# Performance work log

Hardware: AMD Instinct MI355X
Metric: run time of the kernel (lower is better)

The kernel has to match this reference:

```python
import jax, jax.numpy as jnp
import numpy as np


def setup_inputs() -> dict:
    key = jax.random.key(0)
    ks = jax.random.split(key, 5)
    B, S, D, L = 16, 256, 768, 32
    return {
        "head": jax.random.normal(ks[0], (B, S, D), dtype=jnp.float32),
        "dep": jax.random.normal(ks[1], (B, S, D), dtype=jnp.float32),
        "label_U_diag": jax.random.normal(ks[2], (L, D), dtype=jnp.float32) * 0.02,
        "label_W": jax.random.normal(ks[3], (L, 2 * D), dtype=jnp.float32) * 0.02,
        "label_b": jax.random.normal(ks[4], (L,), dtype=jnp.float32) * 0.02,
    }


def reference(head, dep, label_U_diag, label_W, label_b):
    # head, dep: [b, s, d]; label_U_diag: [l, d]; label_W: [l, 2d]; label_b: [l]
    d = head.shape[-1]
    # Bilinear term with diagonal U: t1[b,l,i,o] = sum_d head[b,i,d]*U[l,d]*dep[b,o,d]
    t1 = jnp.einsum('bid,ld,bod->blio', head, label_U_diag, dep)
    # Linear term: W @ concat(head_i, dep_o) = W_h @ head_i + W_d @ dep_o
    W_h, W_d = label_W[:, :d], label_W[:, d:]
    t2_h = jnp.einsum('ld,bid->bli', W_h, head)  # [b, l, s]
    t2_d = jnp.einsum('ld,bod->blo', W_d, dep)   # [b, l, s]
    return t1 + t2_h[:, :, :, None] + t2_d[:, :, None, :] + label_b[None, :, None, None]
```

## Files before the change

kernel.cpp:

```cpp
#include <hip/hip_runtime.h>
#include <hip/hip_bf16.h>
#include <stdint.h>


#define B_ 16
#define S_ 256
#define D_ 768
#define L_ 32
#define KQ_ (D_ / 8)
#define NT_ 24

typedef unsigned short ushort_t;
typedef __attribute__((ext_vector_type(4))) float f32x4;
typedef __attribute__((ext_vector_type(8))) short s16x8;

__device__ __forceinline__ unsigned int pack_bf16(float f0, float f1) {
  unsigned int u0 = __builtin_bit_cast(unsigned int, f0) + 0x8000u;
  unsigned int u1 = __builtin_bit_cast(unsigned int, f1) + 0x8000u;
  return __builtin_amdgcn_perm(u1, u0, 0x07060302);
}

__global__ __launch_bounds__(256) void prep_kernel(
    const float* __restrict__ head, const float* __restrict__ dep,
    const float* __restrict__ labelW, ushort_t* __restrict__ depb,
    float* __restrict__ t2h, float* __restrict__ t2d) {
  const int wave = threadIdx.x >> 6;
  const int lane = threadIdx.x & 63;
  const int g = blockIdx.x * 4 + wave;
  const int sel = g >> 10;
  const int idx = g & 1023;
  const int b = idx >> 6;
  const int row0 = (idx & 63) * 4;
  const float* src = sel ? dep : head;
  float* t2x = sel ? t2d : t2h;
  const int d0 = lane * 12;

  float h[4][12];
  const float* rp = src + ((size_t)(b * S_ + row0)) * D_ + d0;
#pragma unroll
  for (int r = 0; r < 4; ++r) {
    float4 v0 = *(const float4*)(rp + (size_t)r * D_);
    float4 v1 = *(const float4*)(rp + (size_t)r * D_ + 4);
    float4 v2 = *(const float4*)(rp + (size_t)r * D_ + 8);
    h[r][0] = v0.x; h[r][1] = v0.y; h[r][2] = v0.z; h[r][3] = v0.w;
    h[r][4] = v1.x; h[r][5] = v1.y; h[r][6] = v1.z; h[r][7] = v1.w;
    h[r][8] = v2.x; h[r][9] = v2.y; h[r][10] = v2.z; h[r][11] = v2.w;
  }
  if (sel) {
    const size_t bb = (size_t)b * (KQ_ * S_ * 8);
    const int m = lane >> 1;
#pragma unroll
    for (int r = 0; r < 4; ++r) {
      const int col = row0 + r;
      unsigned int q0 = pack_bf16(h[r][0], h[r][1]);
      unsigned int q1 = pack_bf16(h[r][2], h[r][3]);
      unsigned int q2 = pack_bf16(h[r][4], h[r][5]);
      unsigned int q3 = pack_bf16(h[r][6], h[r][7]);
      unsigned int q4 = pack_bf16(h[r][8], h[r][9]);
      unsigned int q5 = pack_bf16(h[r][10], h[r][11]);
      if ((lane & 1) == 0) {
        uint4 a = {q0, q1, q2, q3};
        uint2 c = {q4, q5};
        *(uint4*)(depb + bb + ((size_t)(3 * m) * S_ + col) * 8) = a;
        *(uint2*)(depb + bb + ((size_t)(3 * m + 1) * S_ + col) * 8) = c;
      } else {
        uint2 c = {q0, q1};
        uint4 a = {q2, q3, q4, q5};
        *(uint2*)(depb + bb + ((size_t)(3 * m + 1) * S_ + col) * 8 + 4) = c;
        *(uint4*)(depb + bb + ((size_t)(3 * m + 2) * S_ + col) * 8) = a;
      }
    }
  }
  const float* wbase = labelW + sel * D_ + d0;
  for (int c = 0; c < 2; ++c) {
    float v[64];
#pragma unroll
    for (int j = 0; j < 64; ++j) v[j] = 0.f;
    const float* wc = wbase + (size_t)(c * 16) * (2 * D_);
#pragma unroll
    for (int lq = 0; lq < 16; ++lq) {
      const float* wp = wc + (size_t)lq * (2 * D_);
      float4 w0 = *(const float4*)(wp);
      float4 w1 = *(const float4*)(wp + 4);
      float4 w2 = *(const float4*)(wp + 8);
      float w[12] = {w0.x, w0.y, w0.z, w0.w, w1.x, w1.y, w1.z, w1.w,
                     w2.x, w2.y, w2.z, w2.w};
#pragma unroll
      for (int j = 0; j < 12; ++j) {
        v[lq * 4 + 0] += h[0][j] * w[j];
        v[lq * 4 + 1] += h[1][j] * w[j];
        v[lq * 4 + 2] += h[2][j] * w[j];
        v[lq * 4 + 3] += h[3][j] * w[j];
      }
    }
#pragma unroll
    for (int off = 32; off >= 1; off >>= 1) {
      const bool hi = (lane & off) != 0;
#pragma unroll
      for (int k = 0; k < 64; ++k) {
        if (k >= off) continue;
        float send = hi ? v[k] : v[k + off];
        float keep = hi ? v[k + off] : v[k];
        v[k] = keep + __shfl_xor(send, off);
      }
    }
    t2x[((size_t)(b * L_ + c * 16 + (lane >> 2))) * S_ + row0 + (lane & 3)] =
        v[0];
  }
}


#define SWZ(o) ((o) ^ ((((o) >> 10) & 3) << 4))

__global__ __launch_bounds__(256, 3) void main_kernel(
    const float* __restrict__ head, const ushort_t* __restrict__ depb,
    const float* __restrict__ U, const float* __restrict__ bias,
    const float* __restrict__ t2h, const float* __restrict__ t2d,
    float* __restrict__ out) {
  __shared__ __attribute__((aligned(16))) ushort_t As[2 * 128 * 32];
  __shared__ float T2[256];

  const int hw = blockIdx.x;
  const int bid = ((hw & 7) << 8) | (hw >> 3);
  const int oh = bid & 1;
  const int ih = (bid >> 1) & 1;
  const int l = (bid >> 2) & (L_ - 1);
  const int b = bid >> 7;
  const int ti = ih * 128;
  const int to = oh * 128;
  const int t = threadIdx.x;
  const int lane = t & 63;
  const int wave = t >> 6;
  const int m_base = (wave >> 1) * 64;
  const int n_base = (wave & 1) * 64;

  for (int i = t; i < 256; i += 256)
    T2[i] = (i < 128) ? t2h[((size_t)(b * L_ + l)) * S_ + ti + i]
                      : t2d[((size_t)(b * L_ + l)) * S_ + to + (i - 128)];
  const float bv = bias[l];

  const int row0 = t >> 2;
  const int kg = t & 3;
  const float* hp0 = head + ((size_t)(b * S_ + ti + row0)) * D_ + kg * 8;
  const float* hp1 = hp0 + (size_t)64 * D_;
  const float* Up = U + (size_t)l * D_ + kg * 8;
  const int awo0s = SWZ((kg * 128 + row0) * 8);
  const int awo1s = awo0s + 512;

  const int aros = SWZ(((lane >> 4) * 128 + m_base + (lane & 15)) * 8);

  const ushort_t* dfb =
      depb + (size_t)b * (KQ_ * S_ * 8) +
      ((size_t)((lane >> 4) * 256 + to + n_base + (lane & 15))) * 8;

  f32x4 acc[4][4];
#pragma unroll
  for (int i = 0; i < 4; ++i)
#pragma unroll
    for (int j = 0; j < 4; ++j) acc[i][j] = {0.f, 0.f, 0.f, 0.f};

  s16x8 bfA[4], bfB[4];

  {
    float4 h0 = *(const float4*)(hp0);
    float4 h1 = *(const float4*)(hp0 + 4);
    float4 h2 = *(const float4*)(hp1);
    float4 h3 = *(const float4*)(hp1 + 4);
    float4 u0 = *(const float4*)(Up);
    float4 u1 = *(const float4*)(Up + 4);
    uint4 w0, w1;
    w0.x = pack_bf16(h0.x * u0.x, h0.y * u0.y);
    w0.y = pack_bf16(h0.z * u0.z, h0.w * u0.w);
    w0.z = pack_bf16(h1.x * u1.x, h1.y * u1.y);
    w0.w = pack_bf16(h1.z * u1.z, h1.w * u1.w);
    w1.x = pack_bf16(h2.x * u0.x, h2.y * u0.y);
    w1.y = pack_bf16(h2.z * u0.z, h2.w * u0.w);
    w1.z = pack_bf16(h3.x * u1.x, h3.y * u1.y);
    w1.w = pack_bf16(h3.z * u1.z, h3.w * u1.w);
    *(uint4*)(As + awo0s) = w0;
    *(uint4*)(As + awo1s) = w1;
#pragma unroll
    for (int ct = 0; ct < 4; ++ct)
      bfA[ct] = *(const s16x8*)(dfb + ct * 128);
  }
  asm volatile("s_waitcnt lgkmcnt(0)" ::: "memory");
  __builtin_amdgcn_s_barrier();
  __builtin_amdgcn_sched_barrier(0);

#define ITER(PB, BFC, BFN, tcur)                                              \
  {                                                                           \
    int tn = (tcur) + 1;                                                      \
    if (tn == NT_) tn = 0;     \
    const float* hA = hp0 + tn * 32;                                          \
    const float* hB = hp1 + tn * 32;                                          \
    const float* uA = Up + tn * 32;                                           \
    float4 h0 = *(const float4*)(hA);                                         \
    float4 h1 = *(const float4*)(hA + 4);                                     \
    float4 h2 = *(const float4*)(hB);                                         \
    float4 h3 = *(const float4*)(hB + 4);                                     \
    float4 u0 = *(const float4*)(uA);                                         \
    float4 u1 = *(const float4*)(uA + 4);                                     \
    const ushort_t* dfn = dfb + (size_t)tn * 8192;                            \
    _Pragma("unroll") for (int ct = 0; ct < 4; ++ct)                          \
        BFN[ct] = *(const s16x8*)(dfn + ct * 128);                            \
    __builtin_amdgcn_sched_barrier(0);       \
    s16x8 af[4];                                                              \
    _Pragma("unroll") for (int rt = 0; rt < 4; ++rt)                          \
        af[rt] = *(const s16x8*)(As + (PB)*4096 + aros + rt * 128);           \
    _Pragma("unroll") for (int rt = 0; rt < 4; ++rt)                          \
      _Pragma("unroll") for (int ct = 0; ct < 4; ++ct)                        \
          acc[rt][ct] = __builtin_amdgcn_mfma_f32_16x16x32_bf16(              \
              af[rt], BFC[ct], acc[rt][ct], 0, 0, 0);                         \
    uint4 w0, w1;                                                             \
    w0.x = pack_bf16(h0.x * u0.x, h0.y * u0.y);                               \
    w0.y = pack_bf16(h0.z * u0.z, h0.w * u0.w);                               \
    w0.z = pack_bf16(h1.x * u1.x, h1.y * u1.y);                               \
    w0.w = pack_bf16(h1.z * u1.z, h1.w * u1.w);                               \
    w1.x = pack_bf16(h2.x * u0.x, h2.y * u0.y);                               \
    w1.y = pack_bf16(h2.z * u0.z, h2.w * u0.w);                               \
    w1.z = pack_bf16(h3.x * u1.x, h3.y * u1.y);                               \
    w1.w = pack_bf16(h3.z * u1.z, h3.w * u1.w);                               \
    ushort_t* aw = As + ((PB) ^ 1) * 4096;                                    \
    *(uint4*)(aw + awo0s) = w0;                                               \
    *(uint4*)(aw + awo1s) = w1;                                               \
    asm volatile("s_waitcnt lgkmcnt(0)" ::: "memory");                        \
    __builtin_amdgcn_s_barrier();                                             \
    __builtin_amdgcn_sched_barrier(0);                                        \
  }

  for (int tt = 0; tt < NT_; tt += 2) {
    ITER(0, bfA, bfB, tt);
    ITER(1, bfB, bfA, tt + 1);
  }
#undef ITER

  const int colg = lane & 15;
  const int rgrp = lane >> 4;
  float* ob = out + (((size_t)(b * L_ + l)) * S_ + ti) * S_ + to;
#pragma unroll
  for (int rt = 0; rt < 4; ++rt) {
    const int r0 = m_base + rt * 16 + rgrp * 4;
#pragma unroll
    for (int ct = 0; ct < 4; ++ct) {
      const int c = n_base + ct * 16 + colg;
      const float addc = T2[128 + c] + bv;
      float* p = ob + (size_t)r0 * S_ + c;
#pragma unroll
      for (int r = 0; r < 4; ++r)
        p[(size_t)r * S_] = acc[rt][ct][r] + T2[r0 + r] + addc;
    }
  }
}

extern "C" void kernel_launch(void* const* d_in, const int* in_sizes, int n_in,
                              void* d_out, int out_size, void* d_ws, size_t ws_size,
                              hipStream_t stream) {
  const float* head = (const float*)d_in[0];
  const float* dep = (const float*)d_in[1];
  const float* U = (const float*)d_in[2];
  const float* W = (const float*)d_in[3];
  const float* bias = (const float*)d_in[4];
  float* out = (float*)d_out;

  ushort_t* depb = (ushort_t*)d_ws;
  float* t2h = (float*)((char*)d_ws + (size_t)B_ * S_ * D_ * 2);
  float* t2d = t2h + (size_t)B_ * L_ * S_;

  prep_kernel<<<512, 256, 0, stream>>>(head, dep, W, depb, t2h, t2d);
  main_kernel<<<B_ * L_ * 4, 256, 0, stream>>>(head, depb, U, bias, t2h, t2d, out);
}
```

Baseline: 232.9 us.

## Retile main kernel to 64x256 blocks with three k-chunks per barrier

The block tile changes from 128x128 to 64 rows by 256 columns, so all four waves share one 64-row A tile and each wave covers its own 64-column strip of dep. Each shared buffer now holds three 32-wide k-chunks, so a block synchronises 8 times instead of 24, and the head/U prefetch runs three chunks ahead. The aim is fewer barriers and less staging of head*U per output. The cost is more dep traffic per block and a larger shared-memory footprint, with the swizzle adjusted to the new row count.

Result: faster. 224.9 us (-3.4%).

```diff
diff --git a/kernel.cpp b/kernel.cpp
--- a/kernel.cpp
+++ b/kernel.cpp
@@ -8,7 +8,8 @@
 #define D_ 768
 #define L_ 32
 #define KQ_ (D_ / 8)
-#define NT_ 24
+#define NT_ 8
+#define NKT_ 24
 
 typedef unsigned short ushort_t;
 typedef __attribute__((ext_vector_type(4))) float f32x4;
@@ -110,48 +111,42 @@
 }
 
 
-#define SWZ(o) ((o) ^ ((((o) >> 10) & 3) << 4))
+#define SWZ(o) ((o) ^ ((((o) >> 9) & 3) << 4))
 
 __global__ __launch_bounds__(256, 3) void main_kernel(
     const float* __restrict__ head, const ushort_t* __restrict__ depb,
     const float* __restrict__ U, const float* __restrict__ bias,
     const float* __restrict__ t2h, const float* __restrict__ t2d,
     float* __restrict__ out) {
-  __shared__ __attribute__((aligned(16))) ushort_t As[2 * 128 * 32];
-  __shared__ float T2[256];
+  __shared__ __attribute__((aligned(16))) ushort_t As[2 * 3 * 2048];
+  __shared__ float T2[320];
 
   const int hw = blockIdx.x;
   const int bid = ((hw & 7) << 8) | (hw >> 3);
-  const int oh = bid & 1;
-  const int ih = (bid >> 1) & 1;
+  const int rq = bid & 3;
   const int l = (bid >> 2) & (L_ - 1);
   const int b = bid >> 7;
-  const int ti = ih * 128;
-  const int to = oh * 128;
+  const int ti = rq * 64;
   const int t = threadIdx.x;
   const int lane = t & 63;
   const int wave = t >> 6;
-  const int m_base = (wave >> 1) * 64;
-  const int n_base = (wave & 1) * 64;
-
-  for (int i = t; i < 256; i += 256)
-    T2[i] = (i < 128) ? t2h[((size_t)(b * L_ + l)) * S_ + ti + i]
-                      : t2d[((size_t)(b * L_ + l)) * S_ + to + (i - 128)];
+
+  for (int i = t; i < 320; i += 256)
+    T2[i] = (i < 64) ? t2h[((size_t)(b * L_ + l)) * S_ + ti + i]
+                     : t2d[((size_t)(b * L_ + l)) * S_ + (i - 64)];
   const float bv = bias[l];
 
   const int row0 = t >> 2;
   const int kg = t & 3;
-  const float* hp0 = head + ((size_t)(b * S_ + ti + row0)) * D_ + kg * 8;
-  const float* hp1 = hp0 + (size_t)64 * D_;
+  const float* hp = head + ((size_t)(b * S_ + ti + row0)) * D_ + kg * 8;
   const float* Up = U + (size_t)l * D_ + kg * 8;
-  const int awo0s = SWZ((kg * 128 + row0) * 8);
-  const int awo1s = awo0s + 512;
-
-  const int aros = SWZ(((lane >> 4) * 128 + m_base + (lane & 15)) * 8);
+  const int awos = SWZ((kg * 64 + row0) * 8);
+
+  const int aros = SWZ(((lane >> 4) * 64 + (lane & 15)) * 8);
 
   const ushort_t* dfb =
       depb + (size_t)b * (KQ_ * S_ * 8) +
-      ((size_t)((lane >> 4) * 256 + to + n_base + (lane & 15))) * 8;
+      ((size_t)((lane >> 4) * 256 + wave * 64 + (lane & 15))) * 8;
 
   f32x4 acc[4][4];
 #pragma unroll
@@ -161,24 +156,25 @@
 
   s16x8 bfA[4], bfB[4];
 
+#define PACK_WRITE_CH(BUF, PH)                                                \
+  {                                                                           \
+    uint4 w;                                                                  \
+    w.x = pack_bf16(hh0.x * uu0.x, hh0.y * uu0.y);                            \
+    w.y = pack_bf16(hh0.z * uu0.z, hh0.w * uu0.w);                            \
+    w.z = pack_bf16(hh1.x * uu1.x, hh1.y * uu1.y);                            \
+    w.w = pack_bf16(hh1.z * uu1.z, hh1.w * uu1.w);                            \
+    *(uint4*)(As + (BUF)*6144 + (PH)*2048 + awos) = w;                        \
+  }
+
   {
-    float4 h0 = *(const float4*)(hp0);
-    float4 h1 = *(const float4*)(hp0 + 4);
-    float4 h2 = *(const float4*)(hp1);
-    float4 h3 = *(const float4*)(hp1 + 4);
-    float4 u0 = *(const float4*)(Up);
-    float4 u1 = *(const float4*)(Up + 4);
-    uint4 w0, w1;
-    w0.x = pack_bf16(h0.x * u0.x, h0.y * u0.y);
-    w0.y = pack_bf16(h0.z * u0.z, h0.w * u0.w);
-    w0.z = pack_bf16(h1.x * u1.x, h1.y * u1.y);
-    w0.w = pack_bf16(h1.z * u1.z, h1.w * u1.w);
-    w1.x = pack_bf16(h2.x * u0.x, h2.y * u0.y);
-    w1.y = pack_bf16(h2.z * u0.z, h2.w * u0.w);
-    w1.z = pack_bf16(h3.x * u1.x, h3.y * u1.y);
-    w1.w = pack_bf16(h3.z * u1.z, h3.w * u1.w);
-    *(uint4*)(As + awo0s) = w0;
-    *(uint4*)(As + awo1s) = w1;
+#pragma unroll
+    for (int c = 0; c < 3; ++c) {
+      float4 hh0 = *(const float4*)(hp + c * 32);
+      float4 hh1 = *(const float4*)(hp + c * 32 + 4);
+      float4 uu0 = *(const float4*)(Up + c * 32);
+      float4 uu1 = *(const float4*)(Up + c * 32 + 4);
+      PACK_WRITE_CH(0, c)
+    }
 #pragma unroll
     for (int ct = 0; ct < 4; ++ct)
       bfA[ct] = *(const s16x8*)(dfb + ct * 128);
@@ -187,42 +183,37 @@
   __builtin_amdgcn_s_barrier();
   __builtin_amdgcn_sched_barrier(0);
 
-#define ITER(PB, BFC, BFN, tcur)                                              \
+#define PHASE(PB, PH, BFC, BFN, tcur)                                         \
   {                                                                           \
-    int tn = (tcur) + 1;                                                      \
-    if (tn == NT_) tn = 0;     \
-    const float* hA = hp0 + tn * 32;                                          \
-    const float* hB = hp1 + tn * 32;                                          \
-    const float* uA = Up + tn * 32;                                           \
-    float4 h0 = *(const float4*)(hA);                                         \
-    float4 h1 = *(const float4*)(hA + 4);                                     \
-    float4 h2 = *(const float4*)(hB);                                         \
-    float4 h3 = *(const float4*)(hB + 4);                                     \
-    float4 u0 = *(const float4*)(uA);                                         \
-    float4 u1 = *(const float4*)(uA + 4);                                     \
-    const ushort_t* dfn = dfb + (size_t)tn * 8192;                            \
+    const int kt = (tcur)*3 + (PH);                                           \
+    int ktn = kt + 1;                                                         \
+    if (ktn == NKT_) ktn = 0;           \
+    int ku = kt + 3;                                                          \
+    if (ku >= NKT_) ku -= NKT_;                                               \
+    const ushort_t* dfn = dfb + (size_t)ktn * 8192;                           \
     _Pragma("unroll") for (int ct = 0; ct < 4; ++ct)                          \
         BFN[ct] = *(const s16x8*)(dfn + ct * 128);                            \
+    float4 hh0 = *(const float4*)(hp + ku * 32);                              \
+    float4 hh1 = *(const float4*)(hp + ku * 32 + 4);                          \
+    float4 uu0 = *(const float4*)(Up + ku * 32);                              \
+    float4 uu1 = *(const float4*)(Up + ku * 32 + 4);                          \
     __builtin_amdgcn_sched_barrier(0);       \
+    const ushort_t* arb = As + (PB)*6144 + (PH)*2048 + aros;                  \
     s16x8 af[4];                                                              \
     _Pragma("unroll") for (int rt = 0; rt < 4; ++rt)                          \
-        af[rt] = *(const s16x8*)(As + (PB)*4096 + aros + rt * 128);           \
+        af[rt] = *(const s16x8*)(arb + rt * 128);                             \
     _Pragma("unroll") for (int rt = 0; rt < 4; ++rt)                          \
       _Pragma("unroll") for (int ct = 0; ct < 4; ++ct)                        \
           acc[rt][ct] = __builtin_amdgcn_mfma_f32_16x16x32_bf16(              \
               af[rt], BFC[ct], acc[rt][ct], 0, 0, 0);                         \
-    uint4 w0, w1;                                                             \
-    w0.x = pack_bf16(h0.x * u0.x, h0.y * u0.y);                               \
-    w0.y = pack_bf16(h0.z * u0.z, h0.w * u0.w);                               \
-    w0.z = pack_bf16(h1.x * u1.x, h1.y * u1.y);                               \
-    w0.w = pack_bf16(h1.z * u1.z, h1.w * u1.w);                               \
-    w1.x = pack_bf16(h2.x * u0.x, h2.y * u0.y);                               \
-    w1.y = pack_bf16(h2.z * u0.z, h2.w * u0.w);                               \
-    w1.z = pack_bf16(h3.x * u1.x, h3.y * u1.y);                               \
-    w1.w = pack_bf16(h3.z * u1.z, h3.w * u1.w);                               \
-    ushort_t* aw = As + ((PB) ^ 1) * 4096;                                    \
-    *(uint4*)(aw + awo0s) = w0;                                               \
-    *(uint4*)(aw + awo1s) = w1;                                               \
+    PACK_WRITE_CH((PB) ^ 1, PH)                                               \
+  }
+
+#define ITER(PB, BFX, BFY, tcur)                                              \
+  {                                                                           \
+    PHASE(PB, 0, BFX, BFY, tcur)                                              \
+    PHASE(PB, 1, BFY, BFX, tcur)                                              \
+    PHASE(PB, 2, BFX, BFY, tcur)                                              \
     asm volatile("s_waitcnt lgkmcnt(0)" ::: "memory");                        \
     __builtin_amdgcn_s_barrier();                                             \
     __builtin_amdgcn_sched_barrier(0);                                        \
@@ -233,17 +224,19 @@
     ITER(1, bfB, bfA, tt + 1);
   }
 #undef ITER
+#undef PHASE
+#undef PACK_WRITE_CH
 
   const int colg = lane & 15;
   const int rgrp = lane >> 4;
-  float* ob = out + (((size_t)(b * L_ + l)) * S_ + ti) * S_ + to;
+  float* ob = out + (((size_t)(b * L_ + l)) * S_ + ti) * S_;
 #pragma unroll
   for (int rt = 0; rt < 4; ++rt) {
-    const int r0 = m_base + rt * 16 + rgrp * 4;
+    const int r0 = rt * 16 + rgrp * 4;
 #pragma unroll
     for (int ct = 0; ct < 4; ++ct) {
-      const int c = n_base + ct * 16 + colg;
-      const float addc = T2[128 + c] + bv;
+      const int c = wave * 64 + ct * 16 + colg;
+      const float addc = T2[64 + c] + bv;
       float* p = ob + (size_t)r0 * S_ + c;
 #pragma unroll
       for (int r = 0; r < 4; ++r)
```
